# Optimization experiments

Hardware: AMD Instinct MI355X
Metric: run time of the kernel (lower is better)

## Reference

```python
import jax, jax.numpy as jnp
import numpy as np

N_NODES = 12288
N_EDGES = 393216
IN_FEAT = 2000
HID = 64


def setup_inputs() -> dict:
    key = jax.random.key(0)
    ks = jax.random.split(key, 8)
    features = jax.random.normal(ks[0], (N_NODES, IN_FEAT), dtype=jnp.float32)
    edge_weight = jax.random.uniform(ks[1], (N_EDGES, 1), dtype=jnp.float32)
    W1 = jax.random.normal(ks[2], (IN_FEAT, HID), dtype=jnp.float32) * 0.05
    b1 = jnp.zeros((HID,), dtype=jnp.float32)
    W2 = jax.random.normal(ks[3], (HID, HID), dtype=jnp.float32) * 0.05
    b2 = jnp.zeros((HID,), dtype=jnp.float32)
    src = jax.random.randint(ks[4], (N_EDGES,), 0, N_NODES, dtype=jnp.int32)
    dst = jax.random.randint(ks[5], (N_EDGES,), 0, N_NODES, dtype=jnp.int32)
    return {"features": features, "edge_weight": edge_weight, "W1": W1, "b1": b1,
            "W2": W2, "b2": b2, "src": src, "dst": dst}


def _weighted_graph_conv(x, W, b, src, dst, edge_weight, out_norm, in_norm):
    # norm='both': pre-scale by out_degree^-0.5
    h = x * out_norm[:, None]
    h = h @ W                                   # [N, out_feats]
    # gather -> per-edge weight multiply -> scatter-sum (DGL update_all)
    m = h[src] * edge_weight                    # [E, out_feats]
    agg = jax.ops.segment_sum(m, dst, num_segments=x.shape[0])
    # post-scale by in_degree^-0.5, add bias; activation=None
    return agg * in_norm[:, None] + b


def reference(features, edge_weight, W1, b1, W2, b2, src, dst):
    N = features.shape[0]
    ones = jnp.ones((src.shape[0],), dtype=jnp.float32)
    deg_out = jnp.clip(jax.ops.segment_sum(ones, src, num_segments=N), 1.0)
    deg_in = jnp.clip(jax.ops.segment_sum(ones, dst, num_segments=N), 1.0)
    out_norm = deg_out ** -0.5
    in_norm = deg_in ** -0.5
    x = _weighted_graph_conv(features, W1, b1, src, dst, edge_weight, out_norm, in_norm)
    x = _weighted_graph_conv(x, W2, b2, src, dst, edge_weight, out_norm, in_norm)
    # InnerProductDecoder with identity activation (dropout off / eval mode)
    adj_rec = x @ x.T                           # [N, N]
    return (adj_rec, x)
```

## Files before the change

kernel.cpp:

```cpp
#include <hip/hip_runtime.h>

#define N_NODES 12288
#define N_EDGES 393216
#define IN_FEAT 2000
#define HID 64

typedef __bf16 bf16x8 __attribute__((ext_vector_type(8)));
typedef float f32x16 __attribute__((ext_vector_type(16)));

__global__ void prep_kernel(const int* __restrict__ src, const int* __restrict__ dst,
                            float* __restrict__ deg_out, float* __restrict__ deg_in,
                            const float* __restrict__ W1, unsigned int* __restrict__ Wpk) {
    int i = blockIdx.x * blockDim.x + threadIdx.x;
    if (i < IN_FEAT * HID) {
        float w = W1[i];
        __bf16 hb = (__bf16)w;
        __bf16 lb = (__bf16)(w - (float)hb);
        Wpk[i] = (unsigned int)__builtin_bit_cast(unsigned short, hb) |
                 ((unsigned int)__builtin_bit_cast(unsigned short, lb) << 16);
    }
    if (i < N_EDGES) {
        atomicAdd(&deg_out[src[i]], 1.0f);
        atomicAdd(&deg_in[dst[i]], 1.0f);
    }
}

__global__ __launch_bounds__(1024) void scan_kernel(const float* __restrict__ deg_in,
                                                    int* __restrict__ offs,
                                                    int* __restrict__ cur) {
    __shared__ int sh[1024];
    int t = threadIdx.x;
    int base = t * 12;
    int s = 0;
#pragma unroll
    for (int i = 0; i < 12; ++i) s += (int)deg_in[base + i];
    sh[t] = s;
    __syncthreads();
    for (int off = 1; off < 1024; off <<= 1) {
        int v = (t >= off) ? sh[t - off] : 0;
        __syncthreads();
        sh[t] += v;
        __syncthreads();
    }
    int run = sh[t] - s;
#pragma unroll
    for (int i = 0; i < 12; ++i) {
        int c = (int)deg_in[base + i];
        offs[base + i] = run;
        cur[base + i] = run;
        run += c;
    }
    if (t == 1023) offs[N_NODES] = run;
}

__global__ void fill_kernel(const int* __restrict__ dst, const int* __restrict__ src,
                            const float* __restrict__ ew, const float* __restrict__ deg_out,
                            int* __restrict__ cur, int2* __restrict__ edata) {
    int e = blockIdx.x * blockDim.x + threadIdx.x;
    if (e < N_EDGES) {
        int s = src[e];
        int p = atomicAdd(&cur[dst[e]], 1);
        float wp = ew[e] / sqrtf(fmaxf(deg_out[s], 1.0f));
        edata[p] = make_int2(s, __float_as_int(wp));
    }
}

__global__ __launch_bounds__(256) void gemm1_kernel(const float* __restrict__ A,
                                                    const unsigned int* __restrict__ Wpk,
                                                    float* __restrict__ h,
                                                    float* __restrict__ slabs) {
    __shared__ __align__(16) char As[32768];
    int t = threadIdx.x;
    int w = t >> 6, l = t & 63, lr = l & 31, lh = l >> 5;
    int row0 = blockIdx.x * 64;
    int s = blockIdx.y;
    int ksbase = s * 500;
    float* hout = (s == 0) ? h : slabs + (size_t)(s - 1) * N_NODES * HID;
    int col = (w >> 1) * 32 + lr;
    int lrow = (w & 1) * 32 + lr;
    const char* arow = As + lrow * 512;
    int rx = lr & 7;
    f32x16 acc = {};

    for (int tile = 0; tile < 4; ++tile) {
        int k0 = ksbase + tile * 128;
        int kvalid = (tile < 3) ? 128 : 116;
        __syncthreads();
#pragma unroll
        for (int i = 0; i < 8; ++i) {
            int c = t + i * 256;
            int r = c >> 5, u16 = c & 31;
            float4 v = make_float4(0.f, 0.f, 0.f, 0.f);
            if (u16 * 4 < kvalid)
                v = *(const float4*)&A[(size_t)(row0 + r) * IN_FEAT + k0 + u16 * 4];
            int uu = (u16 >> 1) ^ (r & 7);
            *(float4*)(As + r * 512 + uu * 32 + (u16 & 1) * 16) = v;
        }
        __syncthreads();

#pragma unroll
        for (int kk = 0; kk < 8; ++kk) {
            int uu = (kk * 2 + lh) ^ rx;
            float4 a01 = *(const float4*)(arow + uu * 32);
            float4 a23 = *(const float4*)(arow + uu * 32 + 16);
            float af[8] = {a01.x, a01.y, a01.z, a01.w, a23.x, a23.y, a23.z, a23.w};
            bf16x8 ah, al, wh, wl;
#pragma unroll
            for (int j = 0; j < 8; ++j) {
                float v = af[j];
                __bf16 hb = (__bf16)v;
                ah[j] = hb;
                al[j] = (__bf16)(v - (float)hb);
                int k = k0 + kk * 16 + lh * 8 + j;
                int kc = (k < IN_FEAT) ? k : 0;
                unsigned int wj = Wpk[kc * HID + col];
                wh[j] = __builtin_bit_cast(__bf16, (unsigned short)(wj & 0xffff));
                wl[j] = __builtin_bit_cast(__bf16, (unsigned short)(wj >> 16));
            }
            acc = __builtin_amdgcn_mfma_f32_32x32x16_bf16(ah, wh, acc, 0, 0, 0);
            acc = __builtin_amdgcn_mfma_f32_32x32x16_bf16(ah, wl, acc, 0, 0, 0);
            acc = __builtin_amdgcn_mfma_f32_32x32x16_bf16(al, wh, acc, 0, 0, 0);
        }
    }
#pragma unroll
    for (int r = 0; r < 16; ++r) {
        int orow = row0 + (w & 1) * 32 + (r & 3) + 8 * (r >> 2) + 4 * lh;
        hout[orow * HID + col] = acc[r];
    }
}

__global__ __launch_bounds__(256) void hreduce_kernel(float* __restrict__ h,
                                                      const float* __restrict__ slabs) {
    int g = blockIdx.x * blockDim.x + threadIdx.x;
    float4 a = ((const float4*)h)[g];
    float4 b = ((const float4*)(slabs))[g];
    float4 c = ((const float4*)(slabs + (size_t)N_NODES * HID))[g];
    float4 d = ((const float4*)(slabs + (size_t)2 * N_NODES * HID))[g];
    a.x += b.x + c.x + d.x;
    a.y += b.y + c.y + d.y;
    a.z += b.z + c.z + d.z;
    a.w += b.w + c.w + d.w;
    ((float4*)h)[g] = a;
}

__global__ __launch_bounds__(256) void layer1_kernel(const float* __restrict__ h,
                                                     const int2* __restrict__ edata,
                                                     const int* __restrict__ offs,
                                                     const float* __restrict__ deg_in,
                                                     const float* __restrict__ b1,
                                                     const float* __restrict__ W2,
                                                     float* __restrict__ h2) {
    __shared__ float Ws[64 * 64];
    __shared__ float xrow[4][64];
    int t = threadIdx.x;
#pragma unroll
    for (int i = 0; i < 16; ++i) Ws[t + i * 256] = W2[t + i * 256];

    int w = t >> 6;
    int n = blockIdx.x * 4 + w;
    int f = t & 63;
    float acc = 0.f;
    int beg = offs[n], end = offs[n + 1];
    int p = beg;
    for (; p + 4 <= end; p += 4) {
        int2 e0 = edata[p];
        int2 e1 = edata[p + 1];
        int2 e2 = edata[p + 2];
        int2 e3 = edata[p + 3];
        float h0 = h[(size_t)e0.x * HID + f];
        float h1 = h[(size_t)e1.x * HID + f];
        float h2v = h[(size_t)e2.x * HID + f];
        float h3 = h[(size_t)e3.x * HID + f];
        acc = fmaf(h0, __int_as_float(e0.y), acc);
        acc = fmaf(h1, __int_as_float(e1.y), acc);
        acc = fmaf(h2v, __int_as_float(e2.y), acc);
        acc = fmaf(h3, __int_as_float(e3.y), acc);
    }
    for (; p < end; ++p) {
        int2 e = edata[p];
        acc = fmaf(h[(size_t)e.x * HID + f], __int_as_float(e.y), acc);
    }
    float in_norm = 1.0f / sqrtf(fmaxf(deg_in[n], 1.0f));
    float x1 = acc * in_norm + b1[f];

    __syncthreads();
    xrow[w][f] = x1;
    float acc2 = 0.f;
#pragma unroll 16
    for (int k = 0; k < 64; ++k)
        acc2 = fmaf(xrow[w][k], Ws[k * 64 + f], acc2);
    h2[n * HID + f] = acc2;
}

__global__ __launch_bounds__(256) void gather2_kernel(const float* __restrict__ h,
                                                      const int2* __restrict__ edata,
                                                      const int* __restrict__ offs,
                                                      const float* __restrict__ deg_in,
                                                      const float* __restrict__ b2,
                                                      float* __restrict__ x_out,
                                                      __bf16* __restrict__ xh,
                                                      __bf16* __restrict__ xl) {
    int n = blockIdx.x * 4 + (threadIdx.x >> 6);
    int f = threadIdx.x & 63;
    float acc = 0.f;
    int beg = offs[n], end = offs[n + 1];
    int p = beg;
    for (; p + 4 <= end; p += 4) {
        int2 e0 = edata[p];
        int2 e1 = edata[p + 1];
        int2 e2 = edata[p + 2];
        int2 e3 = edata[p + 3];
        float h0 = h[(size_t)e0.x * HID + f];
        float h1 = h[(size_t)e1.x * HID + f];
        float h2 = h[(size_t)e2.x * HID + f];
        float h3 = h[(size_t)e3.x * HID + f];
        acc = fmaf(h0, __int_as_float(e0.y), acc);
        acc = fmaf(h1, __int_as_float(e1.y), acc);
        acc = fmaf(h2, __int_as_float(e2.y), acc);
        acc = fmaf(h3, __int_as_float(e3.y), acc);
    }
    for (; p < end; ++p) {
        int2 e = edata[p];
        acc = fmaf(h[(size_t)e.x * HID + f], __int_as_float(e.y), acc);
    }
    float in_norm = 1.0f / sqrtf(fmaxf(deg_in[n], 1.0f));
    float x = acc * in_norm + b2[f];
    int g = n * HID + f;
    x_out[g] = x;
    __bf16 hb = (__bf16)x;
    xh[g] = hb;
    xl[g] = (__bf16)(x - (float)hb);
}

__global__ __launch_bounds__(256) void adj_kernel(const __bf16* __restrict__ xh,
                                                  const __bf16* __restrict__ xl,
                                                  float* __restrict__ adj) {
    __shared__ __align__(16) char Bh[16384];
    __shared__ __align__(16) char Bl[16384];
    int t = threadIdx.x;
    int w = t >> 6, l = t & 63;
    int lr = l & 31, lh = l >> 5;
    int i0 = blockIdx.y * 128 + w * 32;
    int j0 = blockIdx.x * 128;

    const char* gh = (const char*)(xh + (size_t)j0 * HID);
    const char* gl = (const char*)(xl + (size_t)j0 * HID);
#pragma unroll
    for (int i = 0; i < 4; ++i) {
        int c = t + i * 256;
        int row = c >> 3, cin = c & 7;
        int dst = row * 128 + ((cin ^ (row & 7)) << 4);
        *(float4*)(Bh + dst) = *(const float4*)(gh + c * 16);
        *(float4*)(Bl + dst) = *(const float4*)(gl + c * 16);
    }

    const __bf16* arow_h = xh + (size_t)(i0 + lr) * HID + lh * 8;
    const __bf16* arow_l = xl + (size_t)(i0 + lr) * HID + lh * 8;
    bf16x8 ah[4], al[4];
#pragma unroll
    for (int kc = 0; kc < 4; ++kc) {
        ah[kc] = *(const bf16x8*)(arow_h + kc * 16);
        al[kc] = *(const bf16x8*)(arow_l + kc * 16);
    }
    __syncthreads();

#pragma unroll
    for (int ct = 0; ct < 4; ++ct) {
        int row = ct * 32 + lr;
        int rbase = row * 128, rxx = row & 7;
        bf16x8 bh[4], bl[4];
#pragma unroll
        for (int kc = 0; kc < 4; ++kc) {
            int off = rbase + (((kc * 2 + lh) ^ rxx) << 4);
            bh[kc] = *(const bf16x8*)(Bh + off);
            bl[kc] = *(const bf16x8*)(Bl + off);
        }
        f32x16 acc = {};
        acc = __builtin_amdgcn_mfma_f32_32x32x16_bf16(ah[0], bh[0], acc, 0, 0, 0);
        acc = __builtin_amdgcn_mfma_f32_32x32x16_bf16(ah[1], bh[1], acc, 0, 0, 0);
        acc = __builtin_amdgcn_mfma_f32_32x32x16_bf16(ah[2], bh[2], acc, 0, 0, 0);
        acc = __builtin_amdgcn_mfma_f32_32x32x16_bf16(ah[3], bh[3], acc, 0, 0, 0);
        acc = __builtin_amdgcn_mfma_f32_32x32x16_bf16(ah[0], bl[0], acc, 0, 0, 0);
        acc = __builtin_amdgcn_mfma_f32_32x32x16_bf16(ah[1], bl[1], acc, 0, 0, 0);
        acc = __builtin_amdgcn_mfma_f32_32x32x16_bf16(ah[2], bl[2], acc, 0, 0, 0);
        acc = __builtin_amdgcn_mfma_f32_32x32x16_bf16(ah[3], bl[3], acc, 0, 0, 0);
        acc = __builtin_amdgcn_mfma_f32_32x32x16_bf16(al[0], bh[0], acc, 0, 0, 0);
        acc = __builtin_amdgcn_mfma_f32_32x32x16_bf16(al[1], bh[1], acc, 0, 0, 0);
        acc = __builtin_amdgcn_mfma_f32_32x32x16_bf16(al[2], bh[2], acc, 0, 0, 0);
        acc = __builtin_amdgcn_mfma_f32_32x32x16_bf16(al[3], bh[3], acc, 0, 0, 0);

#pragma unroll
        for (int r = 0; r < 16; ++r) {
            int rrow = (r & 3) + 8 * (r >> 2) + 4 * lh;
            adj[(size_t)(i0 + rrow) * N_NODES + j0 + ct * 32 + lr] = acc[r];
        }
    }
}

extern "C" void kernel_launch(void* const* d_in, const int* in_sizes, int n_in,
                              void* d_out, int out_size, void* d_ws, size_t ws_size,
                              hipStream_t stream) {
    const float* features = (const float*)d_in[0];
    const float* ew       = (const float*)d_in[1];
    const float* W1       = (const float*)d_in[2];
    const float* b1       = (const float*)d_in[3];
    const float* W2       = (const float*)d_in[4];
    const float* b2       = (const float*)d_in[5];
    const int*   src      = (const int*)d_in[6];
    const int*   dst      = (const int*)d_in[7];

    float* out   = (float*)d_out;
    float* x_out = out + (size_t)N_NODES * N_NODES;

    const size_t NH = (size_t)N_NODES * HID;
    float* ws      = (float*)d_ws;
    float* deg_out = ws;
    float* deg_in  = ws + N_NODES;
    float* h       = ws + 2 * N_NODES;
    float* slabs   = h + NH;
    int*   offs    = (int*)(slabs + 3 * NH);
    int*   cur     = offs + N_NODES + 1;
    int2*  edata   = (int2*)(cur + N_NODES + 1);
    unsigned int* Wpk = (unsigned int*)(edata + N_EDGES);
    float* h2      = (float*)(Wpk + IN_FEAT * HID);
    __bf16* xh     = (__bf16*)slabs;
    __bf16* xl     = xh + NH;

    hipMemsetAsync(ws, 0, (size_t)(2 * N_NODES) * sizeof(float), stream);

    prep_kernel<<<N_EDGES / 256, 256, 0, stream>>>(src, dst, deg_out, deg_in, W1, Wpk);
    scan_kernel<<<1, 1024, 0, stream>>>(deg_in, offs, cur);
    fill_kernel<<<N_EDGES / 256, 256, 0, stream>>>(dst, src, ew, deg_out, cur, edata);

    gemm1_kernel<<<dim3(N_NODES / 64, 4), 256, 0, stream>>>(features, Wpk, h, slabs);
    hreduce_kernel<<<(N_NODES * HID / 4) / 256, 256, 0, stream>>>(h, slabs);

    layer1_kernel<<<N_NODES / 4, 256, 0, stream>>>(h, edata, offs, deg_in, b1, W2, h2);

    gather2_kernel<<<N_NODES / 4, 256, 0, stream>>>(h2, edata, offs, deg_in, b2, x_out, xh, xl);

    adj_kernel<<<dim3(N_NODES / 128, N_NODES / 128), 256, 0, stream>>>(xh, xl, out);
}
```

Before: 282.3 us.

## Fuse degree scan into prep via last-block, merge fill with split-K GEMM using atomics

Fuses the degree-count kernel with the prefix scan, using a last-block-done counter so the final block performs the scan. It also merges the edge-fill kernel and the split-K GEMM1 into one launch distinguished by block index, which lets the two run concurrently. The split-K partial sums are now accumulated into a zeroed h buffer with float atomics, which removes the slab buffers and the separate reduction kernel. This cuts several launches and some memory traffic, at the cost of a larger memset, atomic contention, and a non-deterministic summation order in h.

After: 352.4 us. +24.8%, slower.

```diff
diff --git a/kernel.cpp b/kernel.cpp
--- a/kernel.cpp
+++ b/kernel.cpp
@@ -8,10 +8,16 @@
 typedef __bf16 bf16x8 __attribute__((ext_vector_type(8)));
 typedef float f32x16 __attribute__((ext_vector_type(16)));
 
-__global__ void prep_kernel(const int* __restrict__ src, const int* __restrict__ dst,
-                            float* __restrict__ deg_out, float* __restrict__ deg_in,
-                            const float* __restrict__ W1, unsigned int* __restrict__ Wpk) {
-    int i = blockIdx.x * blockDim.x + threadIdx.x;
+__global__ __launch_bounds__(256) void build_kernel(const int* __restrict__ src,
+                                                    const int* __restrict__ dst,
+                                                    const float* __restrict__ W1,
+                                                    float* __restrict__ deg_out,
+                                                    float* __restrict__ deg_in,
+                                                    unsigned int* __restrict__ Wpk,
+                                                    int* __restrict__ counter,
+                                                    int* __restrict__ offs,
+                                                    int* __restrict__ cur) {
+    int i = blockIdx.x * 256 + threadIdx.x;
     if (i < IN_FEAT * HID) {
         float w = W1[i];
         __bf16 hb = (__bf16)w;
@@ -19,24 +25,32 @@
         Wpk[i] = (unsigned int)__builtin_bit_cast(unsigned short, hb) |
                  ((unsigned int)__builtin_bit_cast(unsigned short, lb) << 16);
     }
-    if (i < N_EDGES) {
-        atomicAdd(&deg_out[src[i]], 1.0f);
-        atomicAdd(&deg_in[dst[i]], 1.0f);
-    }
-}
-
-__global__ __launch_bounds__(1024) void scan_kernel(const float* __restrict__ deg_in,
-                                                    int* __restrict__ offs,
-                                                    int* __restrict__ cur) {
-    __shared__ int sh[1024];
+    atomicAdd(&deg_out[src[i]], 1.0f);
+    atomicAdd(&deg_in[dst[i]], 1.0f);
+
+    __threadfence();
+    __shared__ int is_last;
+    if (threadIdx.x == 0)
+        is_last = (atomicAdd(counter, 1) == (int)gridDim.x - 1);
+    __syncthreads();
+    if (!is_last) return;
+    __threadfence();
+
+    __shared__ int sh[256];
     int t = threadIdx.x;
-    int base = t * 12;
+    int base = t * 48;
+    int cnt[48];
     int s = 0;
 #pragma unroll
-    for (int i = 0; i < 12; ++i) s += (int)deg_in[base + i];
+    for (int k = 0; k < 48; ++k) {
+        float d = __hip_atomic_load(&deg_in[base + k], __ATOMIC_RELAXED,
+                                    __HIP_MEMORY_SCOPE_AGENT);
+        cnt[k] = (int)d;
+        s += cnt[k];
+    }
     sh[t] = s;
     __syncthreads();
-    for (int off = 1; off < 1024; off <<= 1) {
+    for (int off = 1; off < 256; off <<= 1) {
         int v = (t >= off) ? sh[t - off] : 0;
         __syncthreads();
         sh[t] += v;
@@ -44,38 +58,37 @@
     }
     int run = sh[t] - s;
 #pragma unroll
-    for (int i = 0; i < 12; ++i) {
-        int c = (int)deg_in[base + i];
-        offs[base + i] = run;
-        cur[base + i] = run;
-        run += c;
-    }
-    if (t == 1023) offs[N_NODES] = run;
-}
-
-__global__ void fill_kernel(const int* __restrict__ dst, const int* __restrict__ src,
-                            const float* __restrict__ ew, const float* __restrict__ deg_out,
-                            int* __restrict__ cur, int2* __restrict__ edata) {
-    int e = blockIdx.x * blockDim.x + threadIdx.x;
-    if (e < N_EDGES) {
+    for (int k = 0; k < 48; ++k) {
+        offs[base + k] = run;
+        cur[base + k] = run;
+        run += cnt[k];
+    }
+    if (t == 255) offs[N_NODES] = run;
+}
+
+__global__ __launch_bounds__(256) void work_kernel(const float* __restrict__ A,
+                                                   const unsigned int* __restrict__ Wpk,
+                                                   float* __restrict__ h,
+                                                   const int* __restrict__ dst,
+                                                   const int* __restrict__ src,
+                                                   const float* __restrict__ ew,
+                                                   const float* __restrict__ deg_out,
+                                                   int* __restrict__ cur,
+                                                   int2* __restrict__ edata) {
+    __shared__ __align__(16) char As[32768];
+    int bx = blockIdx.x;
+    if (bx >= 768) {
+        int e = (bx - 768) * 256 + threadIdx.x;
         int s = src[e];
         int p = atomicAdd(&cur[dst[e]], 1);
         float wp = ew[e] / sqrtf(fmaxf(deg_out[s], 1.0f));
         edata[p] = make_int2(s, __float_as_int(wp));
-    }
-}
-
-__global__ __launch_bounds__(256) void gemm1_kernel(const float* __restrict__ A,
-                                                    const unsigned int* __restrict__ Wpk,
-                                                    float* __restrict__ h,
-                                                    float* __restrict__ slabs) {
-    __shared__ __align__(16) char As[32768];
+        return;
+    }
     int t = threadIdx.x;
     int w = t >> 6, l = t & 63, lr = l & 31, lh = l >> 5;
-    int row0 = blockIdx.x * 64;
-    int s = blockIdx.y;
-    int ksbase = s * 500;
-    float* hout = (s == 0) ? h : slabs + (size_t)(s - 1) * N_NODES * HID;
+    int row0 = (bx >> 2) * 64;
+    int ksbase = (bx & 3) * 500;
     int col = (w >> 1) * 32 + lr;
     int lrow = (w & 1) * 32 + lr;
     const char* arow = As + lrow * 512;
@@ -125,22 +138,8 @@
 #pragma unroll
     for (int r = 0; r < 16; ++r) {
         int orow = row0 + (w & 1) * 32 + (r & 3) + 8 * (r >> 2) + 4 * lh;
-        hout[orow * HID + col] = acc[r];
-    }
-}
-
-__global__ __launch_bounds__(256) void hreduce_kernel(float* __restrict__ h,
-                                                      const float* __restrict__ slabs) {
-    int g = blockIdx.x * blockDim.x + threadIdx.x;
-    float4 a = ((const float4*)h)[g];
-    float4 b = ((const float4*)(slabs))[g];
-    float4 c = ((const float4*)(slabs + (size_t)N_NODES * HID))[g];
-    float4 d = ((const float4*)(slabs + (size_t)2 * N_NODES * HID))[g];
-    a.x += b.x + c.x + d.x;
-    a.y += b.y + c.y + d.y;
-    a.z += b.z + c.z + d.z;
-    a.w += b.w + c.w + d.w;
-    ((float4*)h)[g] = a;
+        atomicAdd(&h[orow * HID + col], acc[r]);
+    }
 }
 
 __global__ __launch_bounds__(256) void layer1_kernel(const float* __restrict__ h,
@@ -316,24 +315,23 @@
     float* ws      = (float*)d_ws;
     float* deg_out = ws;
     float* deg_in  = ws + N_NODES;
-    float* h       = ws + 2 * N_NODES;
-    float* slabs   = h + NH;
-    int*   offs    = (int*)(slabs + 3 * NH);
+    int*   counter = (int*)(ws + 2 * N_NODES);
+    float* h       = ws + 2 * N_NODES + 16;
+    int*   offs    = (int*)(h + NH);
     int*   cur     = offs + N_NODES + 1;
     int2*  edata   = (int2*)(cur + N_NODES + 1);
     unsigned int* Wpk = (unsigned int*)(edata + N_EDGES);
-    float* h2      = (float*)(Wpk + IN_FEAT * HID);
-    __bf16* xh     = (__bf16*)slabs;
+    float* h2      = (float*)(Wpk + IN_FEAT * HID + 2);
+    __bf16* xh     = (__bf16*)(h2 + NH);
     __bf16* xl     = xh + NH;
 
-    hipMemsetAsync(ws, 0, (size_t)(2 * N_NODES) * sizeof(float), stream);
-
-    prep_kernel<<<N_EDGES / 256, 256, 0, stream>>>(src, dst, deg_out, deg_in, W1, Wpk);
-    scan_kernel<<<1, 1024, 0, stream>>>(deg_in, offs, cur);
-    fill_kernel<<<N_EDGES / 256, 256, 0, stream>>>(dst, src, ew, deg_out, cur, edata);
-
-    gemm1_kernel<<<dim3(N_NODES / 64, 4), 256, 0, stream>>>(features, Wpk, h, slabs);
-    hreduce_kernel<<<(N_NODES * HID / 4) / 256, 256, 0, stream>>>(h, slabs);
+    hipMemsetAsync(ws, 0, (size_t)(2 * N_NODES + 16 + NH) * sizeof(float), stream);
+
+    build_kernel<<<N_EDGES / 256, 256, 0, stream>>>(src, dst, W1, deg_out, deg_in,
+                                                    Wpk, counter, offs, cur);
+
+    work_kernel<<<768 + N_EDGES / 256, 256, 0, stream>>>(features, Wpk, h,
+                                                         dst, src, ew, deg_out, cur, edata);
 
     layer1_kernel<<<N_NODES / 4, 256, 0, stream>>>(h, edata, offs, deg_in, b1, W2, h2);
 
```
